# Optimization experiments

Measured on AMD Instinct MI355X. Metric: run time of the kernel, lower is better.

The kernel has to match this reference:

```python
import jax, jax.numpy as jnp
import numpy as np

B, S, LQ = 32, 1024, 128
EMB = 256; H = 256; NH = 8; DH = H // NH
NCATE, NCONT, NNODE = 4, 8, 4
VOCAB = 50000
EPS = 1e-5
LK = S - LQ


def _ln(x, g, b):
    mu = jnp.mean(x, -1, keepdims=True)
    xc = x - mu
    var = jnp.mean(xc * xc, -1, keepdims=True)
    return xc * jax.lax.rsqrt(var + EPS) * g + b


def _leaky(x):
    return jnp.where(x >= 0, x, 0.01 * x)  # LeakyReLU slope 0.01 (torch default)


def setup_inputs() -> dict:
    key = jax.random.key(0)
    ks = jax.random.split(key, 48)
    rnd = lambda i, shape, scale=0.02: jax.random.normal(ks[i], shape, dtype=jnp.float32) * scale
    rng = np.random.default_rng(0)
    qidx = jnp.asarray(np.sort(rng.choice(S, LQ, replace=False)).astype(np.int64))
    cate_table = rnd(6, (VOCAB, EMB)).at[0].set(0.0)  # padding_idx=0
    inp = {
        "node": jax.random.normal(ks[0], (B, S, EMB * NNODE), dtype=jnp.float32),
        "cate": jax.random.randint(ks[1], (B, S, NCATE), 0, VOCAB),
        "cont": jax.random.normal(ks[2], (B, S, NCONT), dtype=jnp.float32),
        "query_index": qidx,
        "mask": jax.random.bernoulli(ks[3], 0.1, (B, LK)),
        "cate_table": cate_table,
        "pos_emb": rnd(4, (1, S, H)),
        "node_W": rnd(5, (EMB * NNODE, H)), "node_b": jnp.zeros((H,), jnp.float32),
        "node_ln_g": jnp.ones((H,), jnp.float32), "node_ln_b": jnp.zeros((H,), jnp.float32),
        "cate_W": rnd(7, (EMB * NCATE, H)), "cate_b": jnp.zeros((H,), jnp.float32),
        "cate_ln_g": jnp.ones((H,), jnp.float32), "cate_ln_b": jnp.zeros((H,), jnp.float32),
        "bn_g": jnp.ones((NCONT,), jnp.float32), "bn_b": jnp.zeros((NCONT,), jnp.float32),
        "cont_W": rnd(8, (NCONT, H)), "cont_b": jnp.zeros((H,), jnp.float32),
        "cont_ln_g": jnp.ones((H,), jnp.float32), "cont_ln_b": jnp.zeros((H,), jnp.float32),
        "comb_W": rnd(9, (3 * H, H)), "comb_b": jnp.zeros((H,), jnp.float32),
        "comb_ln_g": jnp.ones((H,), jnp.float32), "comb_ln_b": jnp.zeros((H,), jnp.float32),
        "q_W": rnd(10, (H, H)), "q_b": jnp.zeros((H,), jnp.float32),
        "k_W": rnd(11, (H, H)), "k_b": jnp.zeros((H,), jnp.float32),
        "v_W": rnd(12, (H, H)), "v_b": jnp.zeros((H,), jnp.float32),
        "reg_W1": rnd(13, (H, H)), "reg_b1": jnp.zeros((H,), jnp.float32),
        "reg_ln_g": jnp.ones((H,), jnp.float32), "reg_ln_b": jnp.zeros((H,), jnp.float32),
        "reg_W2": rnd(14, (H, H)), "reg_b2": jnp.zeros((H,), jnp.float32),
    }
    return inp


def reference(node, cate, cont, query_index, mask, cate_table, pos_emb,
              node_W, node_b, node_ln_g, node_ln_b,
              cate_W, cate_b, cate_ln_g, cate_ln_b,
              bn_g, bn_b, cont_W, cont_b, cont_ln_g, cont_ln_b,
              comb_W, comb_b, comb_ln_g, comb_ln_b,
              q_W, q_b, k_W, k_b, v_W, v_b,
              reg_W1, reg_b1, reg_ln_g, reg_ln_b, reg_W2, reg_b2):
    # --- three embedding branches: Linear -> LayerNorm ---
    node_e = _ln(node @ node_W + node_b, node_ln_g, node_ln_b)
    ce = cate_table[cate].reshape(B, S, NCATE * EMB)  # embedding gather
    cate_e = _ln(ce @ cate_W + cate_b, cate_ln_g, cate_ln_b)
    # BatchNorm1d (training-mode batch stats, biased var) over flattened [B*S, C]
    cf = cont.reshape(-1, NCONT)
    mu = jnp.mean(cf, 0)
    var = jnp.mean((cf - mu) ** 2, 0)
    cn = ((cf - mu) * jax.lax.rsqrt(var + EPS) * bn_g + bn_b).reshape(B, S, NCONT)
    cont_e = _ln(cn @ cont_W + cont_b, cont_ln_g, cont_ln_b)
    # --- combine + positions ---
    seq = jnp.concatenate([node_e, cate_e, cont_e], -1)       # [B,S,3H]
    seq = _ln(_leaky(seq) @ comb_W + comb_b, comb_ln_g, comb_ln_b) + pos_emb  # [B,S,H]
    # --- gather-split cross attention: queries vs complement keys ---
    is_q = jnp.zeros((S,), bool).at[query_index].set(True)
    key_index = jnp.nonzero(~is_q, size=LK)[0]                # setdiff1d, static size
    q = seq[:, query_index]                                   # [B,LQ,H]
    kv = seq[:, key_index]                                    # [B,LK,H]
    Q = (q @ q_W + q_b).reshape(B, LQ, NH, DH).transpose(0, 2, 1, 3)
    K = (kv @ k_W + k_b).reshape(B, LK, NH, DH).transpose(0, 2, 1, 3)
    V = (kv @ v_W + v_b).reshape(B, LK, NH, DH).transpose(0, 2, 1, 3)
    scale = jnp.float32(1.0 / np.sqrt(DH))
    scores = jnp.einsum('bhqd,bhkd->bhqk', Q, K) * scale      # [B,NH,LQ,LK]
    scores = jnp.where(mask[:, None, None, :], jnp.float32(-1e9), scores)
    attn = jax.nn.softmax(scores, -1)                         # dropout = identity (eval)
    out = jnp.einsum('bhqk,bhkd->bhqd', attn, V).transpose(0, 2, 1, 3).reshape(B, LQ, H)
    h = _leaky(_ln(out @ reg_W1 + reg_b1, reg_ln_g, reg_ln_b))
    return h @ reg_W2 + reg_b2                                # [B,LQ,H]
```

## Files before the change

kernel.cpp:

```cpp
#include <hip/hip_runtime.h>
#include <cstdint>

#define EPSV 1e-5f
#define AS1 __attribute__((address_space(1)))
#define AS3 __attribute__((address_space(3)))

typedef __attribute__((ext_vector_type(8))) short short8v;
typedef __attribute__((ext_vector_type(4))) float float4v;

__device__ inline unsigned short f2bf(float f) {
    union { float f; unsigned int u; } v; v.f = f;
    unsigned int r = v.u + 0x7FFF + ((v.u >> 16) & 1);
    return (unsigned short)(r >> 16);
}

__device__ inline size_t bidx(int n, int k) {
    return ((size_t)(k >> 5) << 13) + ((size_t)(n >> 4) << 9)
         + (((k >> 3) & 3) << 7) + ((n & 15) << 3) + (k & 7);
}

__device__ inline void gld16(const unsigned short* g, unsigned short* d) {
    __builtin_amdgcn_global_load_lds((const AS1 void*)g, (AS3 void*)d, 16, 0, 0);
}

__device__ inline void issue_b(const unsigned short* Bc, int s, unsigned short* bsb,
                               int w, int l) {
    const unsigned short* g = Bc + ((size_t)s << 13) + (w << 9) + (l << 3);
    unsigned short* d = bsb + (w << 9) + (l << 3);
    #pragma unroll
    for (int i = 0; i < 4; ++i)
        gld16(g + (i << 11), d + (i << 11));
}

__global__ __launch_bounds__(256) void wt_all_k(
    const float* __restrict__ nW, const float* __restrict__ cW, const float* __restrict__ mW,
    const float* __restrict__ qW, const float* __restrict__ kW, const float* __restrict__ vW,
    const float* __restrict__ r1W, const float* __restrict__ r2W,
    unsigned short* __restrict__ nO, unsigned short* __restrict__ cO, unsigned short* __restrict__ mO,
    unsigned short* __restrict__ qO, unsigned short* __restrict__ kO, unsigned short* __restrict__ vO,
    unsigned short* __restrict__ r1O, unsigned short* __restrict__ r2O)
{
    __shared__ float T[64][65];
    int bid = blockIdx.x;
    const float* W; unsigned short* O; int K, tile;
    if (bid < 64)       { W = nW; O = nO; K = 1024; tile = bid; }
    else if (bid < 128) { W = cW; O = cO; K = 1024; tile = bid - 64; }
    else if (bid < 176) { W = mW; O = mO; K = 768;  tile = bid - 128; }
    else {
        int s = (bid - 176) >> 4; tile = (bid - 176) & 15; K = 256;
        switch (s) {
            case 0: W = qW;  O = qO;  break;
            case 1: W = kW;  O = kO;  break;
            case 2: W = vW;  O = vO;  break;
            case 3: W = r1W; O = r1O; break;
            default: W = r2W; O = r2O; break;
        }
    }
    int kTiles = K >> 6;
    int k0 = (tile % kTiles) * 64, n0 = (tile / kTiles) * 64;
    int c = threadIdx.x & 63, r4 = threadIdx.x >> 6;
    #pragma unroll
    for (int rr = 0; rr < 64; rr += 4) {
        int r = rr + r4;
        T[r][c] = W[(size_t)(k0 + r) * 256 + n0 + c];
    }
    __syncthreads();
    #pragma unroll
    for (int rr = 0; rr < 64; rr += 4) {
        int n = rr + r4;
        O[bidx(n0 + n, k0 + c)] = f2bf(T[c][n]);
    }
}

__global__ __launch_bounds__(256) void gemm_nc_k(
    const float* __restrict__ node, const int* __restrict__ cate,
    const float* __restrict__ table,
    const unsigned short* __restrict__ nWt, const unsigned short* __restrict__ cWt,
    const float* __restrict__ nb, const float* __restrict__ cb,
    const float* __restrict__ nlg, const float* __restrict__ nlb,
    const float* __restrict__ clg, const float* __restrict__ clb,
    unsigned short* __restrict__ Y)
{
    __shared__ union UN {
        unsigned short A[2][4096];
        struct { float S[64][4]; float Q[64][4]; } red;
    } U;
    __shared__ unsigned short Bs[2][16384];
    const int t = threadIdx.x;
    const bool isC = blockIdx.x >= 512;
    const int bm = (isC ? (int)blockIdx.x - 512 : (int)blockIdx.x) * 64;
    const int w = t >> 6, l = t & 63, lr = l & 15, lg = l >> 4;
    const int ar = t >> 2;
    const int ac = (t & 3) * 16;
    const int aw0 = (((t & 3) >> 1) << 11) + ((ar >> 4) << 9)
                  + ((((t & 3) * 2) & 3) << 7) + ((ar & 15) << 3);
    const int aw1 = aw0 + 128;

    const unsigned short* Bc = isC ? cWt : nWt;
    const float* bias = isC ? cb : nb;
    const float* lng  = isC ? clg : nlg;
    const float* lnbp = isC ? clb : nlb;
    const int colOff = isC ? 256 : 0;

    const float* apf = node + (size_t)(bm + ar) * 1024 + ac;
    int4 idx4 = {0,0,0,0};
    if (isC) idx4 = *(const int4*)&cate[(bm + ar) * 4];

    float4v acc[4][4];
    #pragma unroll
    for (int i = 0; i < 4; ++i)
        #pragma unroll
        for (int j = 0; j < 4; ++j) acc[i][j] = (float4v)0.f;

    float4 rA[4], rB[4];

    auto loadA = [&](int s, float4 (&r)[4]) {
        const float* p;
        if (isC) {
            int kt = s * 64 + ac;
            int g = kt >> 8;
            int idx = (g == 0) ? idx4.x : (g == 1) ? idx4.y : (g == 2) ? idx4.z : idx4.w;
            p = table + (size_t)idx * 256 + (kt & 255);
        } else {
            p = apf + s * 64;
        }
        #pragma unroll
        for (int i = 0; i < 4; ++i) r[i] = *(const float4*)(p + i * 4);
    };
    auto writeA = [&](const float4 (&r)[4], unsigned short* Ab) {
        short8v v0, v1;
        v0[0] = (short)f2bf(r[0].x); v0[1] = (short)f2bf(r[0].y);
        v0[2] = (short)f2bf(r[0].z); v0[3] = (short)f2bf(r[0].w);
        v0[4] = (short)f2bf(r[1].x); v0[5] = (short)f2bf(r[1].y);
        v0[6] = (short)f2bf(r[1].z); v0[7] = (short)f2bf(r[1].w);
        v1[0] = (short)f2bf(r[2].x); v1[1] = (short)f2bf(r[2].y);
        v1[2] = (short)f2bf(r[2].z); v1[3] = (short)f2bf(r[2].w);
        v1[4] = (short)f2bf(r[3].x); v1[5] = (short)f2bf(r[3].y);
        v1[6] = (short)f2bf(r[3].z); v1[7] = (short)f2bf(r[3].w);
        *(short8v*)&Ab[aw0] = v0;
        *(short8v*)&Ab[aw1] = v1;
    };
    auto comp = [&](const unsigned short* Ab, const unsigned short* bsb) {
        #pragma unroll
        for (int kk = 0; kk < 2; ++kk) {
            short8v af[4], bf[4];
            #pragma unroll
            for (int i = 0; i < 4; ++i)
                af[i] = *(const short8v*)&Ab[kk*2048 + i*512 + lg*128 + lr*8];
            #pragma unroll
            for (int j = 0; j < 4; ++j)
                bf[j] = *(const short8v*)&bsb[kk*8192 + ((w*4 + j) << 9) + (lg << 7) + (lr << 3)];
            #pragma unroll
            for (int i = 0; i < 4; ++i)
                #pragma unroll
                for (int j = 0; j < 4; ++j)
                    acc[i][j] = __builtin_amdgcn_mfma_f32_16x16x32_bf16(af[i], bf[j], acc[i][j], 0, 0, 0);
        }
    };

    issue_b(Bc, 0, &Bs[0][0], w, l);
    issue_b(Bc, 1, &Bs[0][8192], w, l);
    loadA(0, rA);
    for (int s = 0; s < 16; ++s) {
        int cur = s & 1;
        __syncthreads();
        writeA(rA, U.A[cur]);
        __syncthreads();
        if (s + 1 < 16) {
            issue_b(Bc, 2*(s+1),     &Bs[1 - cur][0],    w, l);
            issue_b(Bc, 2*(s+1) + 1, &Bs[1 - cur][8192], w, l);
            loadA(s + 1, rB);
        }
        comp(U.A[cur], &Bs[cur][0]);
        #pragma unroll
        for (int i = 0; i < 4; ++i) rA[i] = rB[i];
    }

    float bv[4];
    #pragma unroll
    for (int j = 0; j < 4; ++j) bv[j] = bias[w*64 + j*16 + lr];
    #pragma unroll
    for (int i = 0; i < 4; ++i)
        #pragma unroll
        for (int j = 0; j < 4; ++j)
            #pragma unroll
            for (int r4 = 0; r4 < 4; ++r4) acc[i][j][r4] += bv[j];

    float ps[4][4], qs[4][4];
    #pragma unroll
    for (int i = 0; i < 4; ++i)
        #pragma unroll
        for (int r4 = 0; r4 < 4; ++r4) {
            float a0 = acc[i][0][r4], a1 = acc[i][1][r4],
                  a2 = acc[i][2][r4], a3 = acc[i][3][r4];
            ps[i][r4] = (a0 + a1) + (a2 + a3);
            qs[i][r4] = (a0*a0 + a1*a1) + (a2*a2 + a3*a3);
        }
    #pragma unroll
    for (int o = 1; o < 16; o <<= 1)
        #pragma unroll
        for (int i = 0; i < 4; ++i)
            #pragma unroll
            for (int r4 = 0; r4 < 4; ++r4) {
                ps[i][r4] += __shfl_xor(ps[i][r4], o);
                qs[i][r4] += __shfl_xor(qs[i][r4], o);
            }
    __syncthreads();
    if (lr == 0) {
        #pragma unroll
        for (int i = 0; i < 4; ++i)
            #pragma unroll
            for (int r4 = 0; r4 < 4; ++r4) {
                U.red.S[i*16 + lg*4 + r4][w] = ps[i][r4];
                U.red.Q[i*16 + lg*4 + r4][w] = qs[i][r4];
            }
    }
    __syncthreads();
    #pragma unroll
    for (int i = 0; i < 4; ++i) {
        float mu[4], rstd[4];
        #pragma unroll
        for (int r4 = 0; r4 < 4; ++r4) {
            int rl = i*16 + lg*4 + r4;
            float s  = (U.red.S[rl][0] + U.red.S[rl][1]) + (U.red.S[rl][2] + U.red.S[rl][3]);
            float qq = (U.red.Q[rl][0] + U.red.Q[rl][1]) + (U.red.Q[rl][2] + U.red.Q[rl][3]);
            float m_ = s * (1.0f/256.0f);
            mu[r4] = m_;
            rstd[r4] = rsqrtf(qq * (1.0f/256.0f) - m_*m_ + EPSV);
        }
        #pragma unroll
        for (int j = 0; j < 4; ++j) {
            int c = w*64 + j*16 + lr;
            float gv = lng[c], b2 = lnbp[c];
            #pragma unroll
            for (int r4 = 0; r4 < 4; ++r4) {
                int row = bm + i*16 + lg*4 + r4;
                float y = (acc[i][j][r4] - mu[r4]) * rstd[r4] * gv + b2;
                y = (y >= 0.f) ? y : 0.01f*y;
                Y[(size_t)row * 768 + colOff + c] = f2bf(y);
            }
        }
    }
}

__global__ __launch_bounds__(256) void gemm_comb_k(
    const unsigned short* __restrict__ A,
    const unsigned short* __restrict__ Bc,
    const float* __restrict__ bias,
    const float* __restrict__ lng, const float* __restrict__ lnbp,
    const float* __restrict__ pos,
    unsigned short* __restrict__ Y)
{
    __shared__ union UC {
        unsigned short A[2][2048];
        struct { float S[32][4]; float Q[32][4]; } red;
    } U;
    __shared__ unsigned short Bs[2][16384];
    const int t = threadIdx.x;
    const int bm = blockIdx.x * 32;
    const int w = t >> 6, l = t & 63, lr = l & 15, lg = l >> 4;
    const int arow = t >> 3;
    const int ake  = (t & 7) * 8;
    const int awo = (((t & 7) >> 2) << 10) + ((arow >> 4) << 9)
                  + (((t & 7) & 3) << 7) + ((arow & 15) << 3);

    const unsigned short* ap = A + (size_t)(bm + arow) * 768 + ake;

    float4v acc[2][4];
    #pragma unroll
    for (int i = 0; i < 2; ++i)
        #pragma unroll
        for (int j = 0; j < 4; ++j) acc[i][j] = (float4v)0.f;

    short8v aA, aB;

    auto comp = [&](const unsigned short* Ab, const unsigned short* bsb) {
        #pragma unroll
        for (int kk = 0; kk < 2; ++kk) {
            short8v af[2], bf[4];
            #pragma unroll
            for (int i = 0; i < 2; ++i)
                af[i] = *(const short8v*)&Ab[kk*1024 + i*512 + lg*128 + lr*8];
            #pragma unroll
            for (int j = 0; j < 4; ++j)
                bf[j] = *(const short8v*)&bsb[kk*8192 + ((w*4 + j) << 9) + (lg << 7) + (lr << 3)];
            #pragma unroll
            for (int i = 0; i < 2; ++i)
                #pragma unroll
                for (int j = 0; j < 4; ++j)
                    acc[i][j] = __builtin_amdgcn_mfma_f32_16x16x32_bf16(af[i], bf[j], acc[i][j], 0, 0, 0);
        }
    };

    issue_b(Bc, 0, &Bs[0][0], w, l);
    issue_b(Bc, 1, &Bs[0][8192], w, l);
    aA = *(const short8v*)(ap);
    for (int s = 0; s < 12; ++s) {
        int cur = s & 1;
        __syncthreads();
        *(short8v*)&U.A[cur][awo] = aA;
        __syncthreads();
        if (s + 1 < 12) {
            issue_b(Bc, 2*(s+1),     &Bs[1 - cur][0],    w, l);
            issue_b(Bc, 2*(s+1) + 1, &Bs[1 - cur][8192], w, l);
            aB = *(const short8v*)(ap + (s + 1) * 64);
        }
        comp(U.A[cur], &Bs[cur][0]);
        aA = aB;
    }

    float bv[4];
    #pragma unroll
    for (int j = 0; j < 4; ++j) bv[j] = bias[w*64 + j*16 + lr];
    #pragma unroll
    for (int i = 0; i < 2; ++i)
        #pragma unroll
        for (int j = 0; j < 4; ++j)
            #pragma unroll
            for (int r4 = 0; r4 < 4; ++r4) acc[i][j][r4] += bv[j];

    float ps[2][4], qs[2][4];
    #pragma unroll
    for (int i = 0; i < 2; ++i)
        #pragma unroll
        for (int r4 = 0; r4 < 4; ++r4) {
            float a0 = acc[i][0][r4], a1 = acc[i][1][r4],
                  a2 = acc[i][2][r4], a3 = acc[i][3][r4];
            ps[i][r4] = (a0 + a1) + (a2 + a3);
            qs[i][r4] = (a0*a0 + a1*a1) + (a2*a2 + a3*a3);
        }
    #pragma unroll
    for (int o = 1; o < 16; o <<= 1)
        #pragma unroll
        for (int i = 0; i < 2; ++i)
            #pragma unroll
            for (int r4 = 0; r4 < 4; ++r4) {
                ps[i][r4] += __shfl_xor(ps[i][r4], o);
                qs[i][r4] += __shfl_xor(qs[i][r4], o);
            }
    __syncthreads();
    if (lr == 0) {
        #pragma unroll
        for (int i = 0; i < 2; ++i)
            #pragma unroll
            for (int r4 = 0; r4 < 4; ++r4) {
                U.red.S[i*16 + lg*4 + r4][w] = ps[i][r4];
                U.red.Q[i*16 + lg*4 + r4][w] = qs[i][r4];
            }
    }
    __syncthreads();
    #pragma unroll
    for (int i = 0; i < 2; ++i) {
        float mu[4], rstd[4];
        #pragma unroll
        for (int r4 = 0; r4 < 4; ++r4) {
            int rl = i*16 + lg*4 + r4;
            float s  = (U.red.S[rl][0] + U.red.S[rl][1]) + (U.red.S[rl][2] + U.red.S[rl][3]);
            float qq = (U.red.Q[rl][0] + U.red.Q[rl][1]) + (U.red.Q[rl][2] + U.red.Q[rl][3]);
            float m_ = s * (1.0f/256.0f);
            mu[r4] = m_;
            rstd[r4] = rsqrtf(qq * (1.0f/256.0f) - m_*m_ + EPSV);
        }
        #pragma unroll
        for (int j = 0; j < 4; ++j) {
            int c = w*64 + j*16 + lr;
            float gv = lng[c], b2 = lnbp[c];
            #pragma unroll
            for (int r4 = 0; r4 < 4; ++r4) {
                int row = bm + i*16 + lg*4 + r4;
                float y = (acc[i][j][r4] - mu[r4]) * rstd[r4] * gv + b2
                        + pos[(size_t)(row & 1023) * 256 + c];
                Y[(size_t)row * 256 + c] = f2bf(y);
            }
        }
    }
}

__global__ __launch_bounds__(256) void gemm_qkv_k(
    const unsigned short* __restrict__ seq,
    const int* __restrict__ qmap, const int* __restrict__ krmap,
    const unsigned short* __restrict__ qWt, const unsigned short* __restrict__ kWt,
    const unsigned short* __restrict__ vWt,
    const float* __restrict__ qb, const float* __restrict__ kb, const float* __restrict__ vb,
    unsigned short* __restrict__ Qo, unsigned short* __restrict__ Ko,
    unsigned short* __restrict__ Vt)
{
    __shared__ unsigned short Asl[2][4096];
    __shared__ unsigned short Bs[2][16384];
    const int t = threadIdx.x;
    const int bid = blockIdx.x;
    int seg, bm;
    const int* gmap; const unsigned short* Bc; const float* bias;
    if (bid < 64)       { seg = 0; bm = bid * 64;         gmap = qmap;  Bc = qWt; bias = qb; }
    else if (bid < 512) { seg = 1; bm = (bid - 64) * 64;  gmap = krmap; Bc = kWt; bias = kb; }
    else                { seg = 2; bm = (bid - 512) * 64; gmap = krmap; Bc = vWt; bias = vb; }
    const int w = t >> 6, l = t & 63, lr = l & 15, lg = l >> 4;
    const int ar = t >> 2;
    const int ac = (t & 3) * 16;
    const int aw0 = (((t & 3) >> 1) << 11) + ((ar >> 4) << 9)
                  + ((((t & 3) * 2) & 3) << 7) + ((ar & 15) << 3);
    const int aw1 = aw0 + 128;

    const unsigned short* ap = seq + (size_t)gmap[bm + ar] * 256 + ac;

    float4v acc[4][4];
    #pragma unroll
    for (int i = 0; i < 4; ++i)
        #pragma unroll
        for (int j = 0; j < 4; ++j) acc[i][j] = (float4v)0.f;

    short8v a0A, a1A, a0B, a1B;

    auto comp = [&](const unsigned short* Ab, const unsigned short* bsb) {
        #pragma unroll
        for (int kk = 0; kk < 2; ++kk) {
            short8v af[4], bf[4];
            #pragma unroll
            for (int i = 0; i < 4; ++i)
                af[i] = *(const short8v*)&Ab[kk*2048 + i*512 + lg*128 + lr*8];
            #pragma unroll
            for (int j = 0; j < 4; ++j)
                bf[j] = *(const short8v*)&bsb[kk*8192 + ((w*4 + j) << 9) + (lg << 7) + (lr << 3)];
            #pragma unroll
            for (int i = 0; i < 4; ++i)
                #pragma unroll
                for (int j = 0; j < 4; ++j)
                    acc[i][j] = __builtin_amdgcn_mfma_f32_16x16x32_bf16(af[i], bf[j], acc[i][j], 0, 0, 0);
        }
    };

    issue_b(Bc, 0, &Bs[0][0], w, l);
    issue_b(Bc, 1, &Bs[0][8192], w, l);
    a0A = *(const short8v*)(ap);
    a1A = *(const short8v*)(ap + 8);
    for (int s = 0; s < 4; ++s) {
        int cur = s & 1;
        __syncthreads();
        *(short8v*)&Asl[cur][aw0] = a0A;
        *(short8v*)&Asl[cur][aw1] = a1A;
        __syncthreads();
        if (s + 1 < 4) {
            issue_b(Bc, 2*(s+1),     &Bs[1 - cur][0],    w, l);
            issue_b(Bc, 2*(s+1) + 1, &Bs[1 - cur][8192], w, l);
            a0B = *(const short8v*)(ap + (s + 1) * 64);
            a1B = *(const short8v*)(ap + (s + 1) * 64 + 8);
        }
        comp(Asl[cur], &Bs[cur][0]);
        a0A = a0B; a1A = a1B;
    }

    float bv[4];
    #pragma unroll
    for (int j = 0; j < 4; ++j) bv[j] = bias[w*64 + j*16 + lr];
    unsigned short* outp = (seg == 0) ? Qo : (seg == 1) ? Ko : Vt;
    #pragma unroll
    for (int i = 0; i < 4; ++i) {
        #pragma unroll
        for (int j = 0; j < 4; ++j) {
            int c = w*64 + j*16 + lr;
            #pragma unroll
            for (int r4 = 0; r4 < 4; ++r4) {
                int rl = i*16 + lg*4 + r4;
                float val = acc[i][j][r4] + bv[j];
                if (seg < 2) {
                    outp[(size_t)(bm + rl) * 256 + c] = f2bf(val);
                } else {
                    int vbk = bm / 896;
                    int kl = bm - vbk * 896 + rl;
                    outp[((size_t)vbk * 256 + c) * 896 + kl] = f2bf(val);
                }
            }
        }
    }
}

template<int EPI>
__global__ __launch_bounds__(256) void gemm_reg_k(
    const unsigned short* __restrict__ Asrc,
    const unsigned short* __restrict__ Bc,
    const float* __restrict__ bias,
    const float* __restrict__ ln_g,
    const float* __restrict__ ln_b,
    void* __restrict__ Cout)
{
    __shared__ union UR {
        unsigned short A[2][4096];
        struct { float S[64][4]; float Q[64][4]; } red;
    } U;
    __shared__ unsigned short Bs[2][16384];
    const int t = threadIdx.x;
    const int bm = blockIdx.x * 64;
    const int w = t >> 6, l = t & 63, lr = l & 15, lg = l >> 4;
    const int ar = t >> 2;
    const int ac = (t & 3) * 16;
    const int aw0 = (((t & 3) >> 1) << 11) + ((ar >> 4) << 9)
                  + ((((t & 3) * 2) & 3) << 7) + ((ar & 15) << 3);
    const int aw1 = aw0 + 128;

    const unsigned short* ap = Asrc + (size_t)(bm + ar) * 256 + ac;

    float4v acc[4][4];
    #pragma unroll
    for (int i = 0; i < 4; ++i)
        #pragma unroll
        for (int j = 0; j < 4; ++j) acc[i][j] = (float4v)0.f;

    short8v a0A, a1A, a0B, a1B;

    auto comp = [&](const unsigned short* Ab, const unsigned short* bsb) {
        #pragma unroll
        for (int kk = 0; kk < 2; ++kk) {
            short8v af[4], bf[4];
            #pragma unroll
            for (int i = 0; i < 4; ++i)
                af[i] = *(const short8v*)&Ab[kk*2048 + i*512 + lg*128 + lr*8];
            #pragma unroll
            for (int j = 0; j < 4; ++j)
                bf[j] = *(const short8v*)&bsb[kk*8192 + ((w*4 + j) << 9) + (lg << 7) + (lr << 3)];
            #pragma unroll
            for (int i = 0; i < 4; ++i)
                #pragma unroll
                for (int j = 0; j < 4; ++j)
                    acc[i][j] = __builtin_amdgcn_mfma_f32_16x16x32_bf16(af[i], bf[j], acc[i][j], 0, 0, 0);
        }
    };

    issue_b(Bc, 0, &Bs[0][0], w, l);
    issue_b(Bc, 1, &Bs[0][8192], w, l);
    a0A = *(const short8v*)(ap);
    a1A = *(const short8v*)(ap + 8);
    for (int s = 0; s < 4; ++s) {
        int cur = s & 1;
        __syncthreads();
        *(short8v*)&U.A[cur][aw0] = a0A;
        *(short8v*)&U.A[cur][aw1] = a1A;
        __syncthreads();
        if (s + 1 < 4) {
            issue_b(Bc, 2*(s+1),     &Bs[1 - cur][0],    w, l);
            issue_b(Bc, 2*(s+1) + 1, &Bs[1 - cur][8192], w, l);
            a0B = *(const short8v*)(ap + (s + 1) * 64);
            a1B = *(const short8v*)(ap + (s + 1) * 64 + 8);
        }
        comp(U.A[cur], &Bs[cur][0]);
        a0A = a0B; a1A = a1B;
    }

    float bv[4];
    #pragma unroll
    for (int j = 0; j < 4; ++j) bv[j] = bias[w*64 + j*16 + lr];
    #pragma unroll
    for (int i = 0; i < 4; ++i)
        #pragma unroll
        for (int j = 0; j < 4; ++j)
            #pragma unroll
            for (int r4 = 0; r4 < 4; ++r4) acc[i][j][r4] += bv[j];

    if (EPI == 0) {
        #pragma unroll
        for (int i = 0; i < 4; ++i)
            #pragma unroll
            for (int j = 0; j < 4; ++j) {
                int c = w*64 + j*16 + lr;
                #pragma unroll
                for (int r4 = 0; r4 < 4; ++r4) {
                    int rl = i*16 + lg*4 + r4;
                    ((float*)Cout)[(size_t)(bm + rl) * 256 + c] = acc[i][j][r4];
                }
            }
    } else {
        float ps[4][4], qs[4][4];
        #pragma unroll
        for (int i = 0; i < 4; ++i)
            #pragma unroll
            for (int r4 = 0; r4 < 4; ++r4) {
                float a0 = acc[i][0][r4], a1 = acc[i][1][r4],
                      a2 = acc[i][2][r4], a3 = acc[i][3][r4];
                ps[i][r4] = (a0 + a1) + (a2 + a3);
                qs[i][r4] = (a0*a0 + a1*a1) + (a2*a2 + a3*a3);
            }
        #pragma unroll
        for (int o = 1; o < 16; o <<= 1)
            #pragma unroll
            for (int i = 0; i < 4; ++i)
                #pragma unroll
                for (int r4 = 0; r4 < 4; ++r4) {
                    ps[i][r4] += __shfl_xor(ps[i][r4], o);
                    qs[i][r4] += __shfl_xor(qs[i][r4], o);
                }
        __syncthreads();
        if (lr == 0) {
            #pragma unroll
            for (int i = 0; i < 4; ++i)
                #pragma unroll
                for (int r4 = 0; r4 < 4; ++r4) {
                    U.red.S[i*16 + lg*4 + r4][w] = ps[i][r4];
                    U.red.Q[i*16 + lg*4 + r4][w] = qs[i][r4];
                }
        }
        __syncthreads();
        #pragma unroll
        for (int i = 0; i < 4; ++i) {
            float mu[4], rstd[4];
            #pragma unroll
            for (int r4 = 0; r4 < 4; ++r4) {
                int rl = i*16 + lg*4 + r4;
                float s  = (U.red.S[rl][0] + U.red.S[rl][1]) + (U.red.S[rl][2] + U.red.S[rl][3]);
                float qq = (U.red.Q[rl][0] + U.red.Q[rl][1]) + (U.red.Q[rl][2] + U.red.Q[rl][3]);
                float m_ = s * (1.0f/256.0f);
                mu[r4] = m_;
                rstd[r4] = rsqrtf(qq * (1.0f/256.0f) - m_*m_ + EPSV);
            }
            #pragma unroll
            for (int j = 0; j < 4; ++j) {
                int c = w*64 + j*16 + lr;
                float gv = ln_g[c], b2 = ln_b[c];
                #pragma unroll
                for (int r4 = 0; r4 < 4; ++r4) {
                    int row = bm + i*16 + lg*4 + r4;
                    float y = (acc[i][j][r4] - mu[r4]) * rstd[r4] * gv + b2;
                    y = (y >= 0.f) ? y : 0.01f*y;
                    ((unsigned short*)Cout)[(size_t)row * 256 + c] = f2bf(y);
                }
            }
        }
    }
}

__global__ __launch_bounds__(256) void bn_stats_k(const float* __restrict__ cont,
                                                  float* __restrict__ stats)
{
    __shared__ float ss[8], sq[8];
    int tid = threadIdx.x;
    if (tid < 8) { ss[tid] = 0.f; sq[tid] = 0.f; }
    __syncthreads();
    int gt = blockIdx.x * 256 + tid;
    float s = 0.f, q = 0.f;
    for (int e = gt; e < 32768*8; e += 256*256) { float v = cont[e]; s += v; q += v*v; }
    int f = gt & 7;
    atomicAdd(&ss[f], s);
    atomicAdd(&sq[f], q);
    __syncthreads();
    if (tid < 8) { atomicAdd(&stats[tid], ss[tid]); atomicAdd(&stats[8+tid], sq[tid]); }
}

__global__ __launch_bounds__(256) void cont_k(
    const float* __restrict__ cont, const float* __restrict__ stats,
    const float* __restrict__ bn_g, const float* __restrict__ bn_b,
    const float* __restrict__ W, const float* __restrict__ bias,
    const float* __restrict__ g, const float* __restrict__ bL,
    unsigned short* __restrict__ seq3)
{
    __shared__ float Ws[8][256];
    __shared__ float sscale[8], sshift[8];
    __shared__ float cr[8];
    __shared__ float red[8];
    int tid = threadIdx.x;
    #pragma unroll
    for (int d = 0; d < 8; ++d) Ws[d][tid] = W[d*256 + tid];
    if (tid < 8) {
        float mean = stats[tid] * (1.0f/32768.0f);
        float var  = stats[8+tid] * (1.0f/32768.0f) - mean*mean;
        float r = rsqrtf(var + EPSV);
        float sc = r * bn_g[tid];
        sscale[tid] = sc;
        sshift[tid] = bn_b[tid] - mean*sc;
    }
    __syncthreads();
    int lane = tid & 63, wv = tid >> 6;
    float gv = g[tid], bv = bL[tid], biasv = bias[tid];
    for (int row = blockIdx.x; row < 32768; row += gridDim.x) {
        if (tid < 8) cr[tid] = cont[(size_t)row*8 + tid]*sscale[tid] + sshift[tid];
        __syncthreads();
        float acc = biasv;
        #pragma unroll
        for (int d = 0; d < 8; ++d) acc += cr[d]*Ws[d][tid];
        float s = acc;
        #pragma unroll
        for (int o = 32; o; o >>= 1) s += __shfl_xor(s, o);
        if (lane == 0) red[wv] = s;
        __syncthreads();
        float mu = (red[0]+red[1]+red[2]+red[3]) * (1.0f/256.0f);
        float dc = acc - mu;
        float qv = dc*dc;
        #pragma unroll
        for (int o = 32; o; o >>= 1) qv += __shfl_xor(qv, o);
        if (lane == 0) red[4+wv] = qv;
        __syncthreads();
        float var = (red[4]+red[5]+red[6]+red[7]) * (1.0f/256.0f);
        float y = dc * rsqrtf(var + EPSV) * gv + bv;
        y = (y >= 0.f) ? y : 0.01f*y;
        seq3[(size_t)row*768 + 512 + tid] = f2bf(y);
        __syncthreads();
    }
}

__global__ void build_maps_k(const int* __restrict__ qidx, int* __restrict__ kmap)
{
    __shared__ int flag[1024];
    __shared__ int scan[1024];
    int t = threadIdx.x;
    flag[t] = 0;
    __syncthreads();
    if (t < 128) flag[qidx[t]] = 1;
    __syncthreads();
    int nq = 1 - flag[t];
    scan[t] = nq;
    __syncthreads();
    for (int off = 1; off < 1024; off <<= 1) {
        int v = (t >= off) ? scan[t - off] : 0;
        __syncthreads();
        scan[t] += v;
        __syncthreads();
    }
    if (nq) kmap[scan[t] - 1] = t;
}

__global__ void expand_maps_k(const int* __restrict__ qidx, const int* __restrict__ kmap,
                              int* __restrict__ qmap, int* __restrict__ krmap)
{
    int i = blockIdx.x * 256 + threadIdx.x;
    if (i < 32*128) { int b = i >> 7; int t = i & 127; qmap[i] = b*1024 + qidx[t]; }
    if (i < 32*896) { int b = i / 896; int t = i - b*896; krmap[i] = b*1024 + kmap[t]; }
}

__global__ __launch_bounds__(256) void mask_sniff_k(const unsigned char* __restrict__ msrc,
                                                    int* __restrict__ flags)
{
    int i = blockIdx.x * 256 + threadIdx.x;
    unsigned char v = msrc[i];
    bool u8  = v && (i & 3);
    bool i32 = v && !(i & 3) && ((i & 7) == 4);
    unsigned long long bu = __ballot(u8);
    unsigned long long bi = __ballot(i32);
    if ((threadIdx.x & 63) == 0) {
        if (bu) atomicOr(&flags[0], 1);
        if (bi) atomicOr(&flags[1], 1);
    }
}

__global__ __launch_bounds__(256) void mask_conv_k(const unsigned char* __restrict__ msrc,
                                                   const int* __restrict__ flags,
                                                   unsigned char* __restrict__ mu8)
{
    int i = blockIdx.x * 256 + threadIdx.x;
    int mode = flags[0] ? 0 : (flags[1] ? 1 : 2);
    unsigned char v;
    if (mode == 0)      v = msrc[i] ? 1 : 0;
    else if (mode == 1) v = ((const int*)msrc)[i] ? 1 : 0;
    else                v = ((const long long*)msrc)[i] ? 1 : 0;
    mu8[i] = v;
}

__global__ __launch_bounds__(256) void attn_mfma_k(
    const unsigned short* __restrict__ Qb,
    const unsigned short* __restrict__ Kb,
    const unsigned short* __restrict__ Vtb,
    const unsigned char* __restrict__ mask,
    unsigned short* __restrict__ out)
{
    __shared__ unsigned short Pw[4][16][72];
    const int t = threadIdx.x;
    const int w = t >> 6, l = t & 63;
    const int lr = l & 15, lg = l >> 4;
    const int bx = blockIdx.x;
    const int qh = bx & 1, h = (bx >> 1) & 7, b = bx >> 4;
    const int qrow0 = b*128 + qh*64 + w*16;

    short8v qf = *(const short8v*)&Qb[(size_t)(qrow0 + lr)*256 + h*32 + lg*8];

    const unsigned short* Kbase = Kb + (size_t)b*896*256 + h*32;
    const unsigned short* Vbase = Vtb + ((size_t)b*256 + h*32)*896;
    const unsigned char* mrow = mask + b*896;

    float4v O0 = (float4v)0.f, O1 = (float4v)0.f;
    float m[4], lsum[4];
    #pragma unroll
    for (int r = 0; r < 4; ++r) { m[r] = -3.0e38f; lsum[r] = 0.f; }

    short8v kf[4], vf[4];
    int mk[4];
    #pragma unroll
    for (int i = 0; i < 4; ++i) {
        kf[i] = *(const short8v*)&Kbase[(size_t)(i*16 + lr)*256 + lg*8];
        mk[i] = mrow[i*16 + lr];
    }
    #pragma unroll
    for (int kc = 0; kc < 2; ++kc)
        #pragma unroll
        for (int nt = 0; nt < 2; ++nt)
            vf[kc*2+nt] = *(const short8v*)&Vbase[(size_t)(nt*16 + lr)*896 + kc*32 + lg*8];

    for (int kt3 = 0; kt3 < 14; ++kt3) {
        const int kb2 = kt3*64 + 64;
        short8v kf2[4], vf2[4];
        int mk2[4];
        if (kt3 < 13) {
            #pragma unroll
            for (int i = 0; i < 4; ++i) {
                kf2[i] = *(const short8v*)&Kbase[(size_t)(kb2 + i*16 + lr)*256 + lg*8];
                mk2[i] = mrow[kb2 + i*16 + lr];
            }
            #pragma unroll
            for (int kc = 0; kc < 2; ++kc)
                #pragma unroll
                for (int nt = 0; nt < 2; ++nt)
                    vf2[kc*2+nt] = *(const short8v*)&Vbase[(size_t)(nt*16 + lr)*896 + kb2 + kc*32 + lg*8];
        }
        float4v s4[4];
        #pragma unroll
        for (int i = 0; i < 4; ++i)
            s4[i] = __builtin_amdgcn_mfma_f32_16x16x32_bf16(qf, kf[i], (float4v)0.f, 0, 0, 0);
        #pragma unroll
        for (int i = 0; i < 4; ++i)
            #pragma unroll
            for (int r = 0; r < 4; ++r)
                s4[i][r] = mk[i] ? -1e9f : s4[i][r] * 0.17677669529663687f;
        float tm[4];
        #pragma unroll
        for (int r = 0; r < 4; ++r)
            tm[r] = fmaxf(fmaxf(s4[0][r], s4[1][r]), fmaxf(s4[2][r], s4[3][r]));
        #pragma unroll
        for (int o = 1; o < 16; o <<= 1)
            #pragma unroll
            for (int r = 0; r < 4; ++r) tm[r] = fmaxf(tm[r], __shfl_xor(tm[r], o));
        float resc[4];
        #pragma unroll
        for (int r = 0; r < 4; ++r) {
            float mn = fmaxf(m[r], tm[r]);
            resc[r] = __expf(m[r] - mn);
            m[r] = mn;
        }
        float rs[4] = {0.f, 0.f, 0.f, 0.f};
        #pragma unroll
        for (int i = 0; i < 4; ++i)
            #pragma unroll
            for (int r = 0; r < 4; ++r) {
                float p = __expf(s4[i][r] - m[r]);
                s4[i][r] = p;
                rs[r] += p;
            }
        #pragma unroll
        for (int o = 1; o < 16; o <<= 1)
            #pragma unroll
            for (int r = 0; r < 4; ++r) rs[r] += __shfl_xor(rs[r], o);
        #pragma unroll
        for (int r = 0; r < 4; ++r) lsum[r] = lsum[r]*resc[r] + rs[r];
        #pragma unroll
        for (int r = 0; r < 4; ++r) { O0[r] *= resc[r]; O1[r] *= resc[r]; }
        #pragma unroll
        for (int i = 0; i < 4; ++i)
            #pragma unroll
            for (int r = 0; r < 4; ++r)
                Pw[w][lg*4 + r][i*16 + lr] = f2bf(s4[i][r]);
        #pragma unroll
        for (int kc = 0; kc < 2; ++kc) {
            short8v pf = *(const short8v*)&Pw[w][lr][kc*32 + lg*8];
            O0 = __builtin_amdgcn_mfma_f32_16x16x32_bf16(pf, vf[kc*2+0], O0, 0, 0, 0);
            O1 = __builtin_amdgcn_mfma_f32_16x16x32_bf16(pf, vf[kc*2+1], O1, 0, 0, 0);
        }
        if (kt3 < 13) {
            #pragma unroll
            for (int i = 0; i < 4; ++i) { kf[i] = kf2[i]; mk[i] = mk2[i]; vf[i] = vf2[i]; }
        }
    }
    #pragma unroll
    for (int r = 0; r < 4; ++r) {
        float inv = 1.0f / lsum[r];
        size_t row = (size_t)(qrow0 + lg*4 + r);
        out[row*256 + h*32 + lr]      = f2bf(O0[r] * inv);
        out[row*256 + h*32 + 16 + lr] = f2bf(O1[r] * inv);
    }
}

extern "C" void kernel_launch(void* const* d_in, const int* in_sizes, int n_in,
                              void* d_out, int out_size, void* d_ws, size_t ws_size,
                              hipStream_t stream)
{
    const float* node       = (const float*)d_in[0];
    const int*   cate       = (const int*)d_in[1];
    const float* cont       = (const float*)d_in[2];
    const int*   qidx       = (const int*)d_in[3];
    const unsigned char* mask = (const unsigned char*)d_in[4];
    const float* cate_table = (const float*)d_in[5];
    const float* pos_emb    = (const float*)d_in[6];
    const float* node_W     = (const float*)d_in[7];
    const float* node_b     = (const float*)d_in[8];
    const float* node_ln_g  = (const float*)d_in[9];
    const float* node_ln_b  = (const float*)d_in[10];
    const float* cate_W     = (const float*)d_in[11];
    const float* cate_b     = (const float*)d_in[12];
    const float* cate_ln_g  = (const float*)d_in[13];
    const float* cate_ln_b  = (const float*)d_in[14];
    const float* bn_g       = (const float*)d_in[15];
    const float* bn_b       = (const float*)d_in[16];
    const float* cont_W     = (const float*)d_in[17];
    const float* cont_b     = (const float*)d_in[18];
    const float* cont_ln_g  = (const float*)d_in[19];
    const float* cont_ln_b  = (const float*)d_in[20];
    const float* comb_W     = (const float*)d_in[21];
    const float* comb_b     = (const float*)d_in[22];
    const float* comb_ln_g  = (const float*)d_in[23];
    const float* comb_ln_b  = (const float*)d_in[24];
    const float* q_W        = (const float*)d_in[25];
    const float* q_b        = (const float*)d_in[26];
    const float* k_W        = (const float*)d_in[27];
    const float* k_b        = (const float*)d_in[28];
    const float* v_W        = (const float*)d_in[29];
    const float* v_b        = (const float*)d_in[30];
    const float* reg_W1     = (const float*)d_in[31];
    const float* reg_b1     = (const float*)d_in[32];
    const float* reg_ln_g   = (const float*)d_in[33];
    const float* reg_ln_b   = (const float*)d_in[34];
    const float* reg_W2     = (const float*)d_in[35];
    const float* reg_b2     = (const float*)d_in[36];

    char* ws = (char*)d_ws;
    unsigned short* seq3bf = (unsigned short*)(ws + 0);
    unsigned short* seqbf  = (unsigned short*)(ws + 83886080);
    unsigned short* Qbf    = (unsigned short*)(ws + 100663296);
    unsigned short* Kbf    = (unsigned short*)(ws + 102760448);
    unsigned short* Vtbf   = (unsigned short*)(ws + 117440512);
    unsigned short* AObf   = (unsigned short*)(ws + 132120576);
    unsigned short* Hbf    = (unsigned short*)(ws + 0);
    float* stats = (float*)(ws + 165675008);
    int*   flags = (int*)  (ws + 165675072);
    int*   kmap  = (int*)  (ws + 165675136);
    int*   qmap  = (int*)  (ws + 165678720);
    int*   krmap = (int*)  (ws + 165695104);
    unsigned char* mu8 = (unsigned char*)(ws + 165809792);
    unsigned short* node_Wt = (unsigned short*)(ws + 165838464);
    unsigned short* cate_Wt = (unsigned short*)(ws + 166362752);
    unsigned short* comb_Wt = (unsigned short*)(ws + 166887040);
    unsigned short* q_Wt    = (unsigned short*)(ws + 167280256);
    unsigned short* k_Wt    = (unsigned short*)(ws + 167411328);
    unsigned short* v_Wt    = (unsigned short*)(ws + 167542400);
    unsigned short* r1_Wt   = (unsigned short*)(ws + 167673472);
    unsigned short* r2_Wt   = (unsigned short*)(ws + 167804544);
    float* outp = (float*)d_out;

    hipMemsetAsync(stats, 0, 128, stream);
    bn_stats_k<<<256, 256, 0, stream>>>(cont, stats);
    mask_sniff_k<<<112, 256, 0, stream>>>(mask, flags);
    mask_conv_k<<<112, 256, 0, stream>>>(mask, flags, mu8);
    wt_all_k<<<256, 256, 0, stream>>>(node_W, cate_W, comb_W, q_W, k_W, v_W, reg_W1, reg_W2,
                                      node_Wt, cate_Wt, comb_Wt, q_Wt, k_Wt, v_Wt, r1_Wt, r2_Wt);

    gemm_nc_k<<<1024, 256, 0, stream>>>(node, cate, cate_table, node_Wt, cate_Wt,
        node_b, cate_b, node_ln_g, node_ln_b, cate_ln_g, cate_ln_b, seq3bf);
    cont_k<<<2048, 256, 0, stream>>>(cont, stats, bn_g, bn_b, cont_W, cont_b,
                                     cont_ln_g, cont_ln_b, seq3bf);
    gemm_comb_k<<<1024, 256, 0, stream>>>(seq3bf, comb_Wt, comb_b,
        comb_ln_g, comb_ln_b, pos_emb, seqbf);
    build_maps_k<<<1, 1024, 0, stream>>>(qidx, kmap);
    expand_maps_k<<<112, 256, 0, stream>>>(qidx, kmap, qmap, krmap);
    gemm_qkv_k<<<960, 256, 0, stream>>>(seqbf, qmap, krmap, q_Wt, k_Wt, v_Wt,
        q_b, k_b, v_b, Qbf, Kbf, Vtbf);
    attn_mfma_k<<<512, 256, 0, stream>>>(Qbf, Kbf, Vtbf, mu8, AObf);
    gemm_reg_k<3><<<64, 256, 0, stream>>>(AObf, r1_Wt, reg_b1, reg_ln_g, reg_ln_b, Hbf);
    gemm_reg_k<0><<<64, 256, 0, stream>>>(Hbf, r2_Wt, reg_b2, nullptr, nullptr, outp);
}
```

Before: 271.2 us.

## Restructure GEMM main loops to one barrier per k-step with deeper A prefetch

Across three GEMM kernels, the main loop now writes the next A tile to the alternate LDS buffer after the MFMA compute. Global loads for A are issued two stages ahead. The two __syncthreads per iteration are replaced with a single barrier that uses a partial vmcnt wait, so outstanding A loads can stay in flight while the async B global-to-LDS copies complete. This aims to cut barrier stalls and hide global latency. The cost is fragile hand-set waitcnt counts that must match the number of outstanding loads for correctness.

Measured after the change: 272.9 us. About the same (+0.6%).

```diff
diff --git a/kernel.cpp b/kernel.cpp
--- a/kernel.cpp
+++ b/kernel.cpp
@@ -4,6 +4,11 @@
 #define EPSV 1e-5f
 #define AS1 __attribute__((address_space(1)))
 #define AS3 __attribute__((address_space(3)))
+
+#define VMCNT_BAR(N) do { \
+    asm volatile("s_waitcnt vmcnt(" #N ") lgkmcnt(0)" ::: "memory"); \
+    __builtin_amdgcn_sched_barrier(0); \
+    __builtin_amdgcn_s_barrier(); } while (0)
 
 typedef __attribute__((ext_vector_type(8))) short short8v;
 typedef __attribute__((ext_vector_type(4))) float float4v;
@@ -112,7 +117,7 @@
         #pragma unroll
         for (int j = 0; j < 4; ++j) acc[i][j] = (float4v)0.f;
 
-    float4 rA[4], rB[4];
+    float4 rA[4];
 
     auto loadA = [&](int s, float4 (&r)[4]) {
         const float* p;
@@ -161,19 +166,28 @@
     issue_b(Bc, 0, &Bs[0][0], w, l);
     issue_b(Bc, 1, &Bs[0][8192], w, l);
     loadA(0, rA);
+    writeA(rA, U.A[0]);
+    loadA(1, rA);
+    asm volatile("s_waitcnt lgkmcnt(0)" ::: "memory");
+    __builtin_amdgcn_sched_barrier(0);
+    __builtin_amdgcn_s_barrier();
+
     for (int s = 0; s < 16; ++s) {
-        int cur = s & 1;
-        __syncthreads();
-        writeA(rA, U.A[cur]);
-        __syncthreads();
+        const int cur = s & 1;
         if (s + 1 < 16) {
             issue_b(Bc, 2*(s+1),     &Bs[1 - cur][0],    w, l);
             issue_b(Bc, 2*(s+1) + 1, &Bs[1 - cur][8192], w, l);
-            loadA(s + 1, rB);
         }
         comp(U.A[cur], &Bs[cur][0]);
-        #pragma unroll
-        for (int i = 0; i < 4; ++i) rA[i] = rB[i];
+        if (s + 1 < 16) {
+            writeA(rA, U.A[1 - cur]);
+            if (s + 2 < 16) {
+                loadA(s + 2, rA);
+                VMCNT_BAR(4);
+            } else {
+                VMCNT_BAR(0);
+            }
+        }
     }
 
     float bv[4];
@@ -272,7 +286,7 @@
         #pragma unroll
         for (int j = 0; j < 4; ++j) acc[i][j] = (float4v)0.f;
 
-    short8v aA, aB;
+    short8v aA;
 
     auto comp = [&](const unsigned short* Ab, const unsigned short* bsb) {
         #pragma unroll
@@ -295,18 +309,28 @@
     issue_b(Bc, 0, &Bs[0][0], w, l);
     issue_b(Bc, 1, &Bs[0][8192], w, l);
     aA = *(const short8v*)(ap);
+    *(short8v*)&U.A[0][awo] = aA;
+    aA = *(const short8v*)(ap + 64);
+    asm volatile("s_waitcnt lgkmcnt(0)" ::: "memory");
+    __builtin_amdgcn_sched_barrier(0);
+    __builtin_amdgcn_s_barrier();
+
     for (int s = 0; s < 12; ++s) {
-        int cur = s & 1;
-        __syncthreads();
-        *(short8v*)&U.A[cur][awo] = aA;
-        __syncthreads();
+        const int cur = s & 1;
         if (s + 1 < 12) {
             issue_b(Bc, 2*(s+1),     &Bs[1 - cur][0],    w, l);
             issue_b(Bc, 2*(s+1) + 1, &Bs[1 - cur][8192], w, l);
-            aB = *(const short8v*)(ap + (s + 1) * 64);
         }
         comp(U.A[cur], &Bs[cur][0]);
-        aA = aB;
+        if (s + 1 < 12) {
+            *(short8v*)&U.A[1 - cur][awo] = aA;
+            if (s + 2 < 12) {
+                aA = *(const short8v*)(ap + (s + 2) * 64);
+                VMCNT_BAR(1);
+            } else {
+                VMCNT_BAR(0);
+            }
+        }
     }
 
     float bv[4];
@@ -409,7 +433,7 @@
         #pragma unroll
         for (int j = 0; j < 4; ++j) acc[i][j] = (float4v)0.f;
 
-    short8v a0A, a1A, a0B, a1B;
+    short8v a0A, a1A;
 
     auto comp = [&](const unsigned short* Ab, const unsigned short* bsb) {
         #pragma unroll
@@ -433,20 +457,32 @@
     issue_b(Bc, 1, &Bs[0][8192], w, l);
     a0A = *(const short8v*)(ap);
     a1A = *(const short8v*)(ap + 8);
+    *(short8v*)&Asl[0][aw0] = a0A;
+    *(short8v*)&Asl[0][aw1] = a1A;
+    a0A = *(const short8v*)(ap + 64);
+    a1A = *(const short8v*)(ap + 72);
+    asm volatile("s_waitcnt lgkmcnt(0)" ::: "memory");
+    __builtin_amdgcn_sched_barrier(0);
+    __builtin_amdgcn_s_barrier();
+
     for (int s = 0; s < 4; ++s) {
-        int cur = s & 1;
-        __syncthreads();
-        *(short8v*)&Asl[cur][aw0] = a0A;
-        *(short8v*)&Asl[cur][aw1] = a1A;
-        __syncthreads();
+        const int cur = s & 1;
         if (s + 1 < 4) {
             issue_b(Bc, 2*(s+1),     &Bs[1 - cur][0],    w, l);
             issue_b(Bc, 2*(s+1) + 1, &Bs[1 - cur][8192], w, l);
-            a0B = *(const short8v*)(ap + (s + 1) * 64);
-            a1B = *(const short8v*)(ap + (s + 1) * 64 + 8);
         }
         comp(Asl[cur], &Bs[cur][0]);
-        a0A = a0B; a1A = a1B;
+        if (s + 1 < 4) {
+            *(short8v*)&Asl[1 - cur][aw0] = a0A;
+            *(short8v*)&Asl[1 - cur][aw1] = a1A;
+            if (s + 2 < 4) {
+                a0A = *(const short8v*)(ap + (s + 2) * 64);
+                a1A = *(const short8v*)(ap + (s + 2) * 64 + 8);
+                VMCNT_BAR(2);
+            } else {
+                VMCNT_BAR(0);
+            }
+        }
     }
 
     float bv[4];
```
